# Kernel optimization log

Hardware: AMD Instinct MI355X
Metric: run time of the kernel (lower is better)

The kernel has to match this reference:

```python
import jax, jax.numpy as jnp
import numpy as np

N_EMBED = 1024
N_HEAD = 16
HEAD_DIM = N_EMBED // N_HEAD


def setup_inputs() -> dict:
    key = jax.random.key(0)
    ks = jax.random.split(key, 5)
    s = 1.0 / np.sqrt(N_EMBED)
    return {
        "x": jax.random.normal(ks[0], (4, 2048, N_EMBED), dtype=jnp.float32),
        "W_kqv": jax.random.normal(ks[1], (3 * N_EMBED, N_EMBED), dtype=jnp.float32) * s,
        "b_kqv": jax.random.normal(ks[2], (3 * N_EMBED,), dtype=jnp.float32) * s,
        "W_proj": jax.random.normal(ks[3], (N_EMBED, N_EMBED), dtype=jnp.float32) * s,
        "b_proj": jax.random.normal(ks[4], (N_EMBED,), dtype=jnp.float32) * s,
    }


def reference(x, W_kqv, b_kqv, W_proj, b_proj):
    B, S, E = x.shape
    H, D = N_HEAD, E // N_HEAD
    kqv = x @ W_kqv.T + b_kqv  # [B,S,3E]
    # torch code splits as k, q, v (in that order)
    k, q, v = jnp.split(kqv, 3, axis=-1)
    to_heads = lambda t: t.reshape(B, S, H, D).transpose(0, 2, 1, 3)  # [B,H,S,D]
    k, q, v = to_heads(k), to_heads(q), to_heads(v)
    scale = 1.0 / np.sqrt(D).astype(np.float32)
    attn = jnp.einsum("bhqd,bhkd->bhqk", q, k) * scale
    causal = jnp.tril(jnp.ones((S, S), dtype=bool))
    attn = jnp.where(causal, attn, -jnp.inf)
    attn = jax.nn.softmax(attn, axis=-1)
    # dropout: eval mode (identity) for deterministic reference
    y = jnp.einsum("bhqk,bhkd->bhqd", attn, v)
    y = y.transpose(0, 2, 1, 3).reshape(B, S, E)
    return y @ W_proj.T + b_proj
```

## Files before the change

kernel.cpp:

```cpp
#include <hip/hip_runtime.h>
#include <cstddef>
#include <cstdint>

#define EMB 1024
#define NH 16
#define HD 64
#define BATCH 4
#define SEQ 2048
#define MROWS (BATCH * SEQ)

typedef __attribute__((ext_vector_type(8))) short bf16x8;
typedef __attribute__((ext_vector_type(4))) float f32x4;

__device__ __forceinline__ unsigned short f2bf(float f) {
    union { float f; unsigned int i; } c; c.f = f;
    return (unsigned short)((c.i + 0x7FFFu + ((c.i >> 16) & 1u)) >> 16);
}
__device__ __forceinline__ unsigned short f2bfr(float f) {
    union { float f; unsigned int i; } c; c.f = f;
    return (unsigned short)((c.i + 0x8000u) >> 16);
}

#define GLOAD_LDS16(gp, lp) __builtin_amdgcn_global_load_lds(                  \
    (const __attribute__((address_space(1))) void*)(gp),                       \
    (__attribute__((address_space(3))) void*)(lp), 16, 0, 0)

__global__ __launch_bounds__(256) void cvt_all(
    const float* __restrict__ x, const float* __restrict__ wk,
    const float* __restrict__ wp, unsigned short* __restrict__ xh,
    unsigned short* __restrict__ wkh, unsigned short* __restrict__ wph) {
    const int A = (BATCH * SEQ * EMB) / 4;
    const int B2 = (3 * EMB * EMB) / 4;
    const int C = (EMB * EMB) / 4;
    const int tot = A + B2 + C;
    const int stride = gridDim.x * blockDim.x;
    for (int i = blockIdx.x * blockDim.x + threadIdx.x; i < tot; i += stride) {
        const float* s; unsigned short* d; int j;
        if (i < A)            { s = x;  d = xh;  j = i; }
        else if (i < A + B2)  { s = wk; d = wkh; j = i - A; }
        else                  { s = wp; d = wph; j = i - A - B2; }
        const float4 v = ((const float4*)s)[j];
        ushort4 h;
        h.x = f2bf(v.x); h.y = f2bf(v.y); h.z = f2bf(v.z); h.w = f2bf(v.w);
        ((ushort4*)d)[j] = h;
    }
}

__device__ __forceinline__ void stage_tile(const unsigned short* __restrict__ src,
                                           int row0, int kt,
                                           unsigned short* lds, int wave, int lane) {
#pragma unroll
    for (int i = 0; i < 2; ++i) {
        const int c = wave * 2 + i;
        const int r = c * 16 + (lane >> 2);
        const int kq = (lane & 3) * 8;
        GLOAD_LDS16(src + (size_t)(row0 + r) * 1024 + kt + kq, lds + c * 512);
    }
}

__global__ __launch_bounds__(256) void gemm_qkv_mfma(
    const unsigned short* __restrict__ xh, const unsigned short* __restrict__ wh,
    const float* __restrict__ bias,
    unsigned short* __restrict__ Ko, unsigned short* __restrict__ Qo,
    unsigned short* __restrict__ Vo) {
    __shared__ unsigned short Ah[128 * 32];
    __shared__ unsigned short Bh[128 * 32];

    const int t = threadIdx.x, lane = t & 63, w = t >> 6;
    const int wr = w >> 1, wc = w & 1;
    const int g8 = (lane >> 4) * 8, g4 = (lane >> 4) * 4, l15 = lane & 15;

    const int nwg = 64 * 24;
    const int lin = blockIdx.x + gridDim.x * blockIdx.y;
    const int swz = (lin & 7) * (nwg >> 3) + (lin >> 3);
    const int m0 = (swz & 63) * 128, n0 = (swz >> 6) * 128;

    f32x4 acc[4][4] = {};

    for (int kt = 0; kt < 1024; kt += 32) {
        stage_tile(xh, m0, kt, Ah, w, lane);
        stage_tile(wh, n0, kt, Bh, w, lane);
        __syncthreads();

        bf16x8 a[4], bb[4];
#pragma unroll
        for (int m = 0; m < 4; ++m)
            a[m] = *(const bf16x8*)&Ah[(wr * 64 + m * 16 + l15) * 32 + g8];
#pragma unroll
        for (int n = 0; n < 4; ++n)
            bb[n] = *(const bf16x8*)&Bh[(wc * 64 + n * 16 + l15) * 32 + g8];
#pragma unroll
        for (int m = 0; m < 4; ++m)
#pragma unroll
            for (int n = 0; n < 4; ++n)
                acc[m][n] = __builtin_amdgcn_mfma_f32_16x16x32_bf16(a[m], bb[n], acc[m][n], 0, 0, 0);
        __syncthreads();
    }

#pragma unroll
    for (int n = 0; n < 4; ++n) {
        const int col = n0 + wc * 64 + n * 16 + l15;
        const float bv = bias[col];
        const int which = col >> 10;
        unsigned short* outp = (which == 0) ? Ko : (which == 1 ? Qo : Vo);
        const int cm = col & 1023, h = cm >> 6, d = cm & 63;
#pragma unroll
        for (int m = 0; m < 4; ++m)
#pragma unroll
            for (int jj = 0; jj < 4; ++jj) {
                const int row = m0 + wr * 64 + m * 16 + g4 + jj;
                const int b = row >> 11, s = row & 2047;
                outp[(((size_t)(b * NH + h) * SEQ + s) << 6) + d] =
                    f2bf(acc[m][n][jj] + bv);
            }
    }
}

__global__ __launch_bounds__(256) void gemm_proj_mfma(
    const unsigned short* __restrict__ Yb, const unsigned short* __restrict__ wh,
    const float* __restrict__ bias, float* __restrict__ Out) {
    __shared__ unsigned short Ah[128 * 32];
    __shared__ unsigned short Bh[128 * 32];

    const int t = threadIdx.x, lane = t & 63, w = t >> 6;
    const int wr = w >> 1, wc = w & 1;
    const int g8 = (lane >> 4) * 8, g4 = (lane >> 4) * 4, l15 = lane & 15;

    const int nwg = 64 * 8;
    const int lin = blockIdx.x + gridDim.x * blockIdx.y;
    const int swz = (lin & 7) * (nwg >> 3) + (lin >> 3);
    const int m0 = (swz & 63) * 128, n0 = (swz >> 6) * 128;

    f32x4 acc[4][4] = {};

    for (int kt = 0; kt < 1024; kt += 32) {
        stage_tile(Yb, m0, kt, Ah, w, lane);
        stage_tile(wh, n0, kt, Bh, w, lane);
        __syncthreads();

        bf16x8 a[4], bb[4];
#pragma unroll
        for (int m = 0; m < 4; ++m)
            a[m] = *(const bf16x8*)&Ah[(wr * 64 + m * 16 + l15) * 32 + g8];
#pragma unroll
        for (int n = 0; n < 4; ++n)
            bb[n] = *(const bf16x8*)&Bh[(wc * 64 + n * 16 + l15) * 32 + g8];
#pragma unroll
        for (int m = 0; m < 4; ++m)
#pragma unroll
            for (int n = 0; n < 4; ++n)
                acc[m][n] = __builtin_amdgcn_mfma_f32_16x16x32_bf16(a[m], bb[n], acc[m][n], 0, 0, 0);
        __syncthreads();
    }

#pragma unroll
    for (int n = 0; n < 4; ++n) {
        const int col = n0 + wc * 64 + n * 16 + l15;
        const float bv = bias[col];
#pragma unroll
        for (int m = 0; m < 4; ++m)
#pragma unroll
            for (int jj = 0; jj < 4; ++jj) {
                const int row = m0 + wr * 64 + m * 16 + g4 + jj;
                Out[(size_t)row * EMB + col] = acc[m][n][jj] + bv;
            }
    }
}

__global__ __launch_bounds__(256, 3) void attn_mfma(
    const unsigned short* __restrict__ Kt, const unsigned short* __restrict__ Qt,
    const unsigned short* __restrict__ Vg, unsigned short* __restrict__ Y) {
    __shared__ unsigned short Ks[128][72];
    __shared__ unsigned short Vs[64][136];
    __shared__ unsigned short Ps[64][136];

    const int lin = blockIdx.x;
    const int swz = (lin & 7) * 128 + (lin >> 3);
    const int pair = swz & 15, bh = swz >> 4;
    const int b = bh >> 4, h = bh & 15;
    const unsigned short* Qp = Qt + ((size_t)bh * SEQ << 6);
    const unsigned short* Kp = Kt + ((size_t)bh * SEQ << 6);
    const unsigned short* Vp = Vg + ((size_t)bh * SEQ << 6);

    const int t = threadIdx.x, lane = t & 63, w = t >> 6;
    const int g8 = (lane >> 4) * 8, g4 = (lane >> 4) * 4, l15 = lane & 15;
    const float SCL = 0.125f * 1.44269504f;

    union U8 { uint4 q; unsigned short u[8]; };
    U8 kreg[4], vreg[4];
    auto loadKV = [&](int tile) {
#pragma unroll
        for (int i = 0; i < 4; ++i) {
            const int c = t + (i << 8);
            const int r = c >> 3, col = (c & 7) * 8;
            kreg[i].q = *(const uint4*)(Kp + ((size_t)tile << 13) + r * 64 + col);
            vreg[i].q = *(const uint4*)(Vp + ((size_t)tile << 13) + r * 64 + col);
        }
    };

#pragma unroll 1
    for (int ph = 0; ph < 2; ++ph) {
        const int qt = ph ? (31 - pair) : pair;
        const int ntiles = (qt >> 1) + 1;
        const int q0 = qt * 64 + w * 16;

        bf16x8 qf[2];
#pragma unroll
        for (int kc = 0; kc < 2; ++kc)
            qf[kc] = *(const bf16x8*)(Qp + ((size_t)(q0 + l15) << 6) + kc * 32 + g8);

        float l_i[4] = {0.f, 0.f, 0.f, 0.f};
        f32x4 o_acc[4] = {};

        loadKV(0);
#pragma unroll 1
        for (int tile = 0; tile < ntiles; ++tile) {
            __syncthreads();
#pragma unroll
            for (int i = 0; i < 4; ++i) {
                const int c = t + (i << 8);
                const int r = c >> 3, col = (c & 7) * 8;
                *(uint4*)&Ks[r][col] = kreg[i].q;
#pragma unroll
                for (int j = 0; j < 8; ++j) {
                    const int d = col + j;
                    Vs[d][r ^ (d & 56)] = vreg[i].u[j];
                }
            }
            if (tile + 1 < ntiles) loadKV(tile + 1);
            __syncthreads();

            f32x4 s[8] = {};
            __builtin_amdgcn_s_setprio(1);
#pragma unroll
            for (int n = 0; n < 8; ++n) {
                const bf16x8 kf0 = *(const bf16x8*)&Ks[n * 16 + l15][g8];
                const bf16x8 kf1 = *(const bf16x8*)&Ks[n * 16 + l15][32 + g8];
                s[n] = __builtin_amdgcn_mfma_f32_16x16x32_bf16(qf[0], kf0, s[n], 0, 0, 0);
                s[n] = __builtin_amdgcn_mfma_f32_16x16x32_bf16(qf[1], kf1, s[n], 0, 0, 0);
            }
            __builtin_amdgcn_s_setprio(0);

            const int kvb = tile << 7;
            auto smx = [&](bool MASK) {
#pragma unroll
                for (int n = 0; n < 8; ++n)
#pragma unroll
                    for (int jj = 0; jj < 4; ++jj) {
                        float v = fmaf(s[n][jj], SCL, -8.0f);
                        if (MASK && (kvb + n * 16 + l15 > q0 + g4 + jj)) v = -1e30f;
                        const float p = exp2f(v);
                        l_i[jj] += p;
                        Ps[w * 16 + g4 + jj][n * 16 + l15] = f2bfr(p);
                    }
            };
            if (tile == ntiles - 1) smx(true); else smx(false);

            __builtin_amdgcn_s_setprio(1);
#pragma unroll
            for (int kc = 0; kc < 4; ++kc) {
                bf16x8 vf[4];
#pragma unroll
                for (int nd = 0; nd < 4; ++nd) {
                    const int d = nd * 16 + l15;
                    vf[nd] = *(const bf16x8*)&Vs[d][(kc * 32 + g8) ^ (d & 56)];
                }
                const bf16x8 pf = *(const bf16x8*)&Ps[w * 16 + l15][kc * 32 + g8];
#pragma unroll
                for (int nd = 0; nd < 4; ++nd)
                    o_acc[nd] = __builtin_amdgcn_mfma_f32_16x16x32_bf16(pf, vf[nd], o_acc[nd], 0, 0, 0);
            }
            __builtin_amdgcn_s_setprio(0);
        }

#pragma unroll
        for (int jj = 0; jj < 4; ++jj) {
            float lv = l_i[jj];
#pragma unroll
            for (int msk = 1; msk < 16; msk <<= 1)
                lv += __shfl_xor(lv, msk, 16);
            const float inv = 1.0f / lv;
            const int srow = q0 + g4 + jj;
#pragma unroll
            for (int nd = 0; nd < 4; ++nd)
                Y[((size_t)(b * SEQ + srow) << 10) + (h << 6) + nd * 16 + l15] =
                    f2bf(o_acc[nd][jj] * inv);
        }
    }
}

extern "C" void kernel_launch(void* const* d_in, const int* in_sizes, int n_in,
                              void* d_out, int out_size, void* d_ws, size_t ws_size,
                              hipStream_t stream) {
    const float* x  = (const float*)d_in[0];
    const float* Wk = (const float*)d_in[1];
    const float* bk = (const float*)d_in[2];
    const float* Wp = (const float*)d_in[3];
    const float* bp = (const float*)d_in[4];
    float* out = (float*)d_out;

    char* ws = (char*)d_ws;
    const size_t MB = 1024 * 1024;
    unsigned short* xh  = (unsigned short*)(ws + 0 * MB);
    unsigned short* wkh = (unsigned short*)(ws + 16 * MB);
    unsigned short* wph = (unsigned short*)(ws + 22 * MB);
    unsigned short* Ko  = (unsigned short*)(ws + 24 * MB);
    unsigned short* Qo  = (unsigned short*)(ws + 40 * MB);
    unsigned short* Vo  = (unsigned short*)(ws + 56 * MB);
    unsigned short* Yo  = (unsigned short*)(ws + 72 * MB);

    cvt_all<<<2048, 256, 0, stream>>>(x, Wk, Wp, xh, wkh, wph);

    gemm_qkv_mfma<<<dim3(MROWS / 128, 3072 / 128), 256, 0, stream>>>(
        xh, wkh, bk, Ko, Qo, Vo);
    attn_mfma<<<1024, 256, 0, stream>>>(Ko, Qo, Vo, Yo);
    gemm_proj_mfma<<<dim3(MROWS / 128, EMB / 128), 256, 0, stream>>>(
        Yo, wph, bp, out);
}
```

Measured before the change: 313.7 us.

## Enlarge attention query tile to 128 rows and compute transposed scores

Each attention block now handles 128 query rows (32 per wave) instead of 64, so each K/V tile staged in shared memory is reused by twice as many queries and no longer wastes half the tile on diagonal masking. The grid is halved to 512 blocks. Scores are computed as K·Q^T so each lane holds consecutive key columns and can write packed bf16 pairs to the P buffer. The row-sum reduction changes to match. The cost is more registers and a larger P buffer, with occupancy lowered to 2 blocks per SIMD group, and fewer blocks to spread across CUs.

```diff
diff --git a/kernel.cpp b/kernel.cpp
--- a/kernel.cpp
+++ b/kernel.cpp
@@ -167,23 +167,23 @@
     }
 }
 
-__global__ __launch_bounds__(256, 3) void attn_mfma(
+__global__ __launch_bounds__(256, 2) void attn_mfma(
     const unsigned short* __restrict__ Kt, const unsigned short* __restrict__ Qt,
     const unsigned short* __restrict__ Vg, unsigned short* __restrict__ Y) {
     __shared__ unsigned short Ks[128][72];
     __shared__ unsigned short Vs[64][136];
-    __shared__ unsigned short Ps[64][136];
+    __shared__ unsigned short Ps[128][136];
 
     const int lin = blockIdx.x;
-    const int swz = (lin & 7) * 128 + (lin >> 3);
-    const int pair = swz & 15, bh = swz >> 4;
+    const int swz = (lin & 7) * 64 + (lin >> 3);
+    const int pair = swz & 7, bh = swz >> 3;
     const int b = bh >> 4, h = bh & 15;
     const unsigned short* Qp = Qt + ((size_t)bh * SEQ << 6);
     const unsigned short* Kp = Kt + ((size_t)bh * SEQ << 6);
     const unsigned short* Vp = Vg + ((size_t)bh * SEQ << 6);
 
     const int t = threadIdx.x, lane = t & 63, w = t >> 6;
-    const int g8 = (lane >> 4) * 8, g4 = (lane >> 4) * 4, l15 = lane & 15;
+    const int hi = lane >> 4, l15 = lane & 15, g8 = hi * 8;
     const float SCL = 0.125f * 1.44269504f;
 
     union U8 { uint4 q; unsigned short u[8]; };
@@ -200,17 +200,20 @@
 
 #pragma unroll 1
     for (int ph = 0; ph < 2; ++ph) {
-        const int qt = ph ? (31 - pair) : pair;
-        const int ntiles = (qt >> 1) + 1;
-        const int q0 = qt * 64 + w * 16;
-
-        bf16x8 qf[2];
-#pragma unroll
-        for (int kc = 0; kc < 2; ++kc)
-            qf[kc] = *(const bf16x8*)(Qp + ((size_t)(q0 + l15) << 6) + kc * 32 + g8);
-
-        float l_i[4] = {0.f, 0.f, 0.f, 0.f};
-        f32x4 o_acc[4] = {};
+        const int qt = ph ? (15 - pair) : pair;
+        const int ntiles = qt + 1;
+        const int q0 = qt * 128 + w * 32;
+
+        bf16x8 qf[2][2];
+#pragma unroll
+        for (int rb = 0; rb < 2; ++rb)
+#pragma unroll
+            for (int kc = 0; kc < 2; ++kc)
+                qf[rb][kc] = *(const bf16x8*)(
+                    Qp + ((size_t)(q0 + rb * 16 + l15) << 6) + kc * 32 + g8);
+
+        float lsum[2] = {0.f, 0.f};
+        f32x4 o_acc[2][4] = {};
 
         loadKV(0);
 #pragma unroll 1
@@ -230,33 +233,43 @@
             if (tile + 1 < ntiles) loadKV(tile + 1);
             __syncthreads();
 
-            f32x4 s[8] = {};
+            const bool diag = (tile == ntiles - 1);
+            const int kvb = tile << 7;
+
             __builtin_amdgcn_s_setprio(1);
 #pragma unroll
             for (int n = 0; n < 8; ++n) {
                 const bf16x8 kf0 = *(const bf16x8*)&Ks[n * 16 + l15][g8];
                 const bf16x8 kf1 = *(const bf16x8*)&Ks[n * 16 + l15][32 + g8];
-                s[n] = __builtin_amdgcn_mfma_f32_16x16x32_bf16(qf[0], kf0, s[n], 0, 0, 0);
-                s[n] = __builtin_amdgcn_mfma_f32_16x16x32_bf16(qf[1], kf1, s[n], 0, 0, 0);
-            }
-            __builtin_amdgcn_s_setprio(0);
-
-            const int kvb = tile << 7;
-            auto smx = [&](bool MASK) {
-#pragma unroll
-                for (int n = 0; n < 8; ++n)
-#pragma unroll
-                    for (int jj = 0; jj < 4; ++jj) {
-                        float v = fmaf(s[n][jj], SCL, -8.0f);
-                        if (MASK && (kvb + n * 16 + l15 > q0 + g4 + jj)) v = -1e30f;
-                        const float p = exp2f(v);
-                        l_i[jj] += p;
-                        Ps[w * 16 + g4 + jj][n * 16 + l15] = f2bfr(p);
+                f32x4 t0 = {}, t1 = {};
+                t0 = __builtin_amdgcn_mfma_f32_16x16x32_bf16(kf0, qf[0][0], t0, 0, 0, 0);
+                t0 = __builtin_amdgcn_mfma_f32_16x16x32_bf16(kf1, qf[0][1], t0, 0, 0, 0);
+                t1 = __builtin_amdgcn_mfma_f32_16x16x32_bf16(kf0, qf[1][0], t1, 0, 0, 0);
+                t1 = __builtin_amdgcn_mfma_f32_16x16x32_bf16(kf1, qf[1][1], t1, 0, 0, 0);
+#pragma unroll
+                for (int rb = 0; rb < 2; ++rb) {
+                    const f32x4 tt = rb ? t1 : t0;
+                    const int qrow = q0 + rb * 16 + l15;
+                    unsigned int pk[2];
+#pragma unroll
+                    for (int jp = 0; jp < 2; ++jp) {
+                        float v0 = fmaf(tt[2 * jp], SCL, -8.0f);
+                        float v1 = fmaf(tt[2 * jp + 1], SCL, -8.0f);
+                        if (diag) {
+                            const int kv = kvb + n * 16 + 4 * hi + 2 * jp;
+                            if (kv > qrow)     v0 = -1e30f;
+                            if (kv + 1 > qrow) v1 = -1e30f;
+                        }
+                        const float p0 = exp2f(v0), p1 = exp2f(v1);
+                        lsum[rb] += p0 + p1;
+                        pk[jp] = (unsigned int)f2bfr(p0) |
+                                 ((unsigned int)f2bfr(p1) << 16);
                     }
-            };
-            if (tile == ntiles - 1) smx(true); else smx(false);
-
-            __builtin_amdgcn_s_setprio(1);
+                    *(uint2*)&Ps[w * 32 + rb * 16 + l15][n * 16 + 4 * hi] =
+                        make_uint2(pk[0], pk[1]);
+                }
+            }
+
 #pragma unroll
             for (int kc = 0; kc < 4; ++kc) {
                 bf16x8 vf[4];
@@ -265,26 +278,31 @@
                     const int d = nd * 16 + l15;
                     vf[nd] = *(const bf16x8*)&Vs[d][(kc * 32 + g8) ^ (d & 56)];
                 }
-                const bf16x8 pf = *(const bf16x8*)&Ps[w * 16 + l15][kc * 32 + g8];
-#pragma unroll
-                for (int nd = 0; nd < 4; ++nd)
-                    o_acc[nd] = __builtin_amdgcn_mfma_f32_16x16x32_bf16(pf, vf[nd], o_acc[nd], 0, 0, 0);
+                const bf16x8 pf0 = *(const bf16x8*)&Ps[w * 32 + l15][kc * 32 + g8];
+                const bf16x8 pf1 = *(const bf16x8*)&Ps[w * 32 + 16 + l15][kc * 32 + g8];
+#pragma unroll
+                for (int nd = 0; nd < 4; ++nd) {
+                    o_acc[0][nd] = __builtin_amdgcn_mfma_f32_16x16x32_bf16(pf0, vf[nd], o_acc[0][nd], 0, 0, 0);
+                    o_acc[1][nd] = __builtin_amdgcn_mfma_f32_16x16x32_bf16(pf1, vf[nd], o_acc[1][nd], 0, 0, 0);
+                }
             }
             __builtin_amdgcn_s_setprio(0);
         }
 
 #pragma unroll
-        for (int jj = 0; jj < 4; ++jj) {
-            float lv = l_i[jj];
-#pragma unroll
-            for (int msk = 1; msk < 16; msk <<= 1)
-                lv += __shfl_xor(lv, msk, 16);
-            const float inv = 1.0f / lv;
-            const int srow = q0 + g4 + jj;
-#pragma unroll
-            for (int nd = 0; nd < 4; ++nd)
-                Y[((size_t)(b * SEQ + srow) << 10) + (h << 6) + nd * 16 + l15] =
-                    f2bf(o_acc[nd][jj] * inv);
+        for (int rb = 0; rb < 2; ++rb) {
+            float lv = lsum[rb];
+            lv += __shfl_xor(lv, 16);
+            lv += __shfl_xor(lv, 32);
+#pragma unroll
+            for (int jj = 0; jj < 4; ++jj) {
+                const float inv = 1.0f / __shfl(lv, 4 * hi + jj);
+                const int srow = q0 + rb * 16 + 4 * hi + jj;
+#pragma unroll
+                for (int nd = 0; nd < 4; ++nd)
+                    Y[((size_t)(b * SEQ + srow) << 10) + (h << 6) + nd * 16 + l15] =
+                        f2bf(o_acc[rb][nd][jj] * inv);
+            }
         }
     }
 }
@@ -313,7 +331,7 @@
 
     gemm_qkv_mfma<<<dim3(MROWS / 128, 3072 / 128), 256, 0, stream>>>(
         xh, wkh, bk, Ko, Qo, Vo);
-    attn_mfma<<<1024, 256, 0, stream>>>(Ko, Qo, Vo, Yo);
+    attn_mfma<<<512, 256, 0, stream>>>(Ko, Qo, Vo, Yo);
     gemm_proj_mfma<<<dim3(MROWS / 128, EMB / 128), 256, 0, stream>>>(
         Yo, wph, bp, out);
 }
```

After: 282.9 us. 1.11x faster.
